# Kernel tuning notes

Measured on AMD Instinct MI355X. Metric: run time of the kernel, lower is better.

The kernel has to match this reference:

```python
import jax, jax.numpy as jnp
import numpy as np

TREE_DEPTH = 6
NUM_TREES = 64
NUM_LEAVES = 2 ** TREE_DEPTH
INPUT_DIM = 256
BATCH = 32768
BN_EPS = 1e-5


def _leaf_codes():
    # [L, depth] binary codes, MSB first (matches format(i, '0{depth}b'))
    i = np.arange(NUM_LEAVES)
    bits = (i[:, None] >> np.arange(TREE_DEPTH - 1, -1, -1)[None, :]) & 1
    return jnp.asarray(bits, dtype=jnp.float32)


def setup_inputs() -> dict:
    key = jax.random.key(0)
    ks = jax.random.split(key, 6)
    s = 1.0 / np.sqrt(INPUT_DIM)
    return {
        "x": jax.random.normal(ks[0], (BATCH, INPUT_DIM), jnp.float32),
        "W_dec": jax.random.normal(ks[1], (NUM_TREES, TREE_DEPTH, INPUT_DIM), jnp.float32) * s,
        "b_dec": jax.random.normal(ks[2], (NUM_TREES, TREE_DEPTH), jnp.float32) * s,
        "leaf_values": jax.random.normal(ks[3], (NUM_TREES, NUM_LEAVES), jnp.float32),
        "bn_gamma": jnp.ones((NUM_TREES,), jnp.float32),
        "bn_beta": jnp.zeros((NUM_TREES,), jnp.float32),
        "bn_mean": jnp.zeros((NUM_TREES,), jnp.float32),
        "bn_var": jnp.ones((NUM_TREES,), jnp.float32),
        "fc_w": jax.random.normal(ks[4], (INPUT_DIM, NUM_TREES), jnp.float32) / np.sqrt(NUM_TREES),
        "fc_b": jnp.zeros((INPUT_DIM,), jnp.float32),
    }


def reference(x, W_dec, b_dec, leaf_values, bn_gamma, bn_beta, bn_mean, bn_var, fc_w, fc_b):
    # Decision probabilities for all trees at once: [B, T, depth]
    dec = jax.nn.sigmoid(jnp.einsum("bd,tkd->btk", x, W_dec) + b_dec)
    codes = _leaf_codes()  # [L, depth]
    # Leaf probabilities: product over depth of (dec*code + (1-dec)*(1-code)).
    # Loop over the small fixed depth to avoid a [B,T,L,depth] intermediate.
    probs = jnp.ones((x.shape[0], NUM_TREES, NUM_LEAVES), x.dtype)
    for d in range(TREE_DEPTH):
        dd = dec[:, :, d][:, :, None]            # [B, T, 1]
        c = codes[:, d]                          # [L]
        probs = probs * (dd * c + (1.0 - dd) * (1.0 - c))
    # Weighted sum of leaf values per tree: [B, T]
    tree_out = jnp.einsum("btl,tl->bt", probs, leaf_values)
    # BatchNorm1d in eval mode (running stats), dropout is identity in eval.
    tree_out = (tree_out - bn_mean) * jax.lax.rsqrt(bn_var + BN_EPS) * bn_gamma + bn_beta
    # Final projection back to input_dim: [B, D]
    return tree_out @ fc_w.T + fc_b
```

## Files before the change

kernel.cpp:

```cpp
#include <hip/hip_runtime.h>
#include <hip/hip_bf16.h>

typedef __attribute__((ext_vector_type(8))) short short8;
typedef __attribute__((ext_vector_type(4))) float floatx4;

#define LOG2E 1.4426950408889634f

__device__ __forceinline__ unsigned short f2bf(float f) {
  unsigned int u = __float_as_uint(f);
  u += 0x7FFFu + ((u >> 16) & 1u);
  return (unsigned short)(u >> 16);
}

__device__ __forceinline__ unsigned int pk2(float lo, float hi) {
  __hip_bfloat162 h = __float22bfloat162_rn(make_float2(lo, hi));
  unsigned int u;
  __builtin_memcpy(&u, &h, 4);
  return u;
}

__global__ void prep_kernel(const float* __restrict__ W_dec,
                            const float* __restrict__ b_dec,
                            const float* __restrict__ leaf,
                            const float* __restrict__ bn_gamma,
                            const float* __restrict__ bn_beta,
                            const float* __restrict__ bn_mean,
                            const float* __restrict__ bn_var,
                            const float* __restrict__ fc_w,
                            unsigned short* __restrict__ Wp,
                            unsigned short* __restrict__ fcw,
                            float* __restrict__ coefg,
                            float* __restrict__ b1)
{
  int idx = (int)blockIdx.x * 256 + (int)threadIdx.x;
  if (idx < 384 * 256) {
    int np = idx >> 8, k = idx & 255;
    int d = np >> 6, t = np & 63;
    Wp[idx] = f2bf(-LOG2E * W_dec[(t * 6 + d) * 256 + k]);
    return;
  }
  idx -= 384 * 256;
  if (idx < 256 * 64) { fcw[idx] = f2bf(fc_w[idx]); return; }
  idx -= 256 * 64;
  if (idx < 64) {
    const int t = idx;
    float c[64];
    #pragma unroll
    for (int i = 0; i < 64; ++i) c[i] = leaf[t * 64 + i];
    #pragma unroll
    for (int p = 0; p < 6; ++p) {
      const int s = 1 << p;
      #pragma unroll
      for (int i = 0; i < 64; ++i)
        if ((i & s) == 0) c[i + s] -= c[i];
    }
    float sbv = bn_gamma[t] * rsqrtf(bn_var[t] + 1e-5f);
    float obv = bn_beta[t] - bn_mean[t] * sbv;
    #pragma unroll
    for (int i = 0; i < 64; ++i) c[i] *= sbv;
    c[0] += obv;
    #pragma unroll
    for (int i = 0; i < 64; ++i) coefg[t * 64 + i] = c[i];
    return;
  }
  idx -= 64;
  if (idx < 384) {
    int t = idx / 6, d = idx % 6;
    b1[d * 64 + t] = -LOG2E * b_dec[idx];
  }
}

__global__ __launch_bounds__(256, 3)
void node_main(const float* __restrict__ x,
               const unsigned short* __restrict__ Wp,
               const unsigned short* __restrict__ fcw,
               const float* __restrict__ coefg,
               const float* __restrict__ b1g,
               const float* __restrict__ fc_b,
               float* __restrict__ out)
{
  __shared__ __align__(16) char smem[36864];
  unsigned short (*xbf)[264] = (unsigned short (*)[264])smem;
  unsigned short (*A2)[72]   = (unsigned short (*)[72])smem;
  float (*coef_lds)[68]      = (float (*)[68])(smem + 16896);
  float* b1_lds              = (float*)(smem + 34304);
  float* fcb_lds             = (float*)(smem + 35840);

  const int tid  = (int)threadIdx.x;
  const int lane = tid & 63;
  const int w    = tid >> 6;
  const int tcol = lane & 15;
  const int g    = lane >> 4;
  const int r0   = (int)blockIdx.x * 32;

  {
    const float4* xs = (const float4*)(x + (size_t)r0 * 256);
    #pragma unroll
    for (int i = 0; i < 8; ++i) {
      int f = tid + 256 * i;
      float4 v = xs[f];
      int row = f >> 6, c4 = f & 63;
      unsigned int* p = (unsigned int*)&xbf[row][c4 * 4];
      p[0] = pk2(v.x, v.y);
      p[1] = pk2(v.z, v.w);
    }
    #pragma unroll
    for (int i = 0; i < 4; ++i) {
      int f = tid + 256 * i;
      int t = f >> 4, c4 = f & 15;
      *(float4*)&coef_lds[t][c4 * 4] = ((const float4*)coefg)[f];
    }
    b1_lds[tid] = b1g[tid];
    if (tid < 128) b1_lds[256 + tid] = b1g[256 + tid];
    fcb_lds[tid] = fc_b[tid];
  }
  __syncthreads();

  floatx4 acc[2][6];
  #pragma unroll
  for (int rt = 0; rt < 2; ++rt)
    #pragma unroll
    for (int d = 0; d < 6; ++d) { acc[rt][d][0]=0.f; acc[rt][d][1]=0.f; acc[rt][d][2]=0.f; acc[rt][d][3]=0.f; }

  const unsigned short* Bb = Wp + (size_t)(w * 16 + tcol) * 256 + g * 8;

  #pragma unroll
  for (int kp = 0; kp < 8; ++kp) {
    short8 b[6];
    #pragma unroll
    for (int d = 0; d < 6; ++d) b[d] = *(const short8*)(Bb + d * 16384 + kp * 32);
    short8 a0 = *(const short8*)&xbf[tcol][kp * 32 + g * 8];
    short8 a1 = *(const short8*)&xbf[16 + tcol][kp * 32 + g * 8];
    #pragma unroll
    for (int d = 0; d < 6; ++d) {
      acc[0][d] = __builtin_amdgcn_mfma_f32_16x16x32_bf16(a0, b[d], acc[0][d], 0, 0, 0);
      acc[1][d] = __builtin_amdgcn_mfma_f32_16x16x32_bf16(a1, b[d], acc[1][d], 0, 0, 0);
    }
  }
  __syncthreads();

  const int tree = w * 16 + tcol;
  float bp[6];
  #pragma unroll
  for (int d = 0; d < 6; ++d) bp[d] = b1_lds[d * 64 + tree];

  #pragma unroll
  for (int rt = 0; rt < 2; ++rt)
    #pragma unroll
    for (int d = 0; d < 6; ++d)
      #pragma unroll
      for (int j = 0; j < 4; ++j) {
        float z = acc[rt][d][j] + bp[d];
        acc[rt][d][j] = __builtin_amdgcn_rcpf(1.0f + __builtin_amdgcn_exp2f(z));
      }

  float L[32], resLo[8];
  #pragma unroll
  for (int c = 0; c < 8; ++c) {
    float4 v = *(const float4*)&coef_lds[tree][c * 4];
    L[c*4+0] = v.x; L[c*4+1] = v.y; L[c*4+2] = v.z; L[c*4+3] = v.w;
  }
  #pragma unroll
  for (int rt = 0; rt < 2; ++rt)
    #pragma unroll
    for (int j = 0; j < 4; ++j) {
      float u[16];
      const float d5 = acc[rt][5][j];
      #pragma unroll
      for (int i = 0; i < 16; ++i) u[i] = fmaf(d5, L[2*i+1], L[2*i]);
      const float d4 = acc[rt][4][j];
      #pragma unroll
      for (int i = 0; i < 8; ++i) u[i] = fmaf(d4, u[2*i+1], u[2*i]);
      const float d3 = acc[rt][3][j];
      #pragma unroll
      for (int i = 0; i < 4; ++i) u[i] = fmaf(d3, u[2*i+1], u[2*i]);
      const float d2 = acc[rt][2][j];
      #pragma unroll
      for (int i = 0; i < 2; ++i) u[i] = fmaf(d2, u[2*i+1], u[2*i]);
      resLo[rt*4+j] = fmaf(acc[rt][1][j], u[1], u[0]);
    }
  #pragma unroll
  for (int c = 0; c < 8; ++c) {
    float4 v = *(const float4*)&coef_lds[tree][32 + c * 4];
    L[c*4+0] = v.x; L[c*4+1] = v.y; L[c*4+2] = v.z; L[c*4+3] = v.w;
  }
  #pragma unroll
  for (int rt = 0; rt < 2; ++rt)
    #pragma unroll
    for (int j = 0; j < 4; ++j) {
      float u[16];
      const float d5 = acc[rt][5][j];
      #pragma unroll
      for (int i = 0; i < 16; ++i) u[i] = fmaf(d5, L[2*i+1], L[2*i]);
      const float d4 = acc[rt][4][j];
      #pragma unroll
      for (int i = 0; i < 8; ++i) u[i] = fmaf(d4, u[2*i+1], u[2*i]);
      const float d3 = acc[rt][3][j];
      #pragma unroll
      for (int i = 0; i < 4; ++i) u[i] = fmaf(d3, u[2*i+1], u[2*i]);
      const float d2 = acc[rt][2][j];
      #pragma unroll
      for (int i = 0; i < 2; ++i) u[i] = fmaf(d2, u[2*i+1], u[2*i]);
      float hi_r = fmaf(acc[rt][1][j], u[1], u[0]);
      float to   = fmaf(acc[rt][0][j], hi_r, resLo[rt*4+j]);
      A2[rt * 16 + g * 4 + j][tree] = f2bf(to);
    }
  __syncthreads();

  floatx4 acc2[2][4];
  #pragma unroll
  for (int rt = 0; rt < 2; ++rt)
    #pragma unroll
    for (int nt = 0; nt < 4; ++nt) { acc2[rt][nt][0]=0.f; acc2[rt][nt][1]=0.f; acc2[rt][nt][2]=0.f; acc2[rt][nt][3]=0.f; }

  #pragma unroll
  for (int kst = 0; kst < 2; ++kst) {
    short8 a2[2];
    #pragma unroll
    for (int rt = 0; rt < 2; ++rt)
      a2[rt] = *(const short8*)&A2[rt * 16 + tcol][kst * 32 + g * 8];
    #pragma unroll
    for (int nt = 0; nt < 4; ++nt) {
      short8 b2 = *(const short8*)(fcw + (size_t)(w * 64 + nt * 16 + tcol) * 64 + kst * 32 + g * 8);
      #pragma unroll
      for (int rt = 0; rt < 2; ++rt)
        acc2[rt][nt] = __builtin_amdgcn_mfma_f32_16x16x32_bf16(a2[rt], b2, acc2[rt][nt], 0, 0, 0);
    }
  }

  #pragma unroll
  for (int nt = 0; nt < 4; ++nt) {
    const int col = w * 64 + nt * 16 + tcol;
    const float bv = fcb_lds[col];
    #pragma unroll
    for (int rt = 0; rt < 2; ++rt)
      #pragma unroll
      for (int j = 0; j < 4; ++j)
        out[(size_t)(r0 + rt * 16 + g * 4 + j) * 256 + col] = acc2[rt][nt][j] + bv;
  }
}

extern "C" void kernel_launch(void* const* d_in, const int* in_sizes, int n_in,
                              void* d_out, int out_size, void* d_ws, size_t ws_size,
                              hipStream_t stream) {
  const float* x        = (const float*)d_in[0];
  const float* W_dec    = (const float*)d_in[1];
  const float* b_dec    = (const float*)d_in[2];
  const float* leaf     = (const float*)d_in[3];
  const float* bn_gamma = (const float*)d_in[4];
  const float* bn_beta  = (const float*)d_in[5];
  const float* bn_mean  = (const float*)d_in[6];
  const float* bn_var   = (const float*)d_in[7];
  const float* fc_w     = (const float*)d_in[8];
  const float* fc_b     = (const float*)d_in[9];
  float* out = (float*)d_out;

  char* ws = (char*)d_ws;
  unsigned short* Wp  = (unsigned short*)(ws);
  unsigned short* fcw = (unsigned short*)(ws + 196608);
  float* coefg = (float*)(ws + 229376);
  float* b1    = (float*)(ws + 245760);

  prep_kernel<<<450, 256, 0, stream>>>(W_dec, b_dec, leaf, bn_gamma, bn_beta,
                                       bn_mean, bn_var, fc_w,
                                       Wp, fcw, coefg, b1);
  node_main<<<1024, 256, 0, stream>>>(x, Wp, fcw, coefg, b1, fc_b, out);
}
```

Before: 45.72 us.

## Double-buffer decision weights into LDS via async global_load_lds and vectorize prep

Decision-weight tiles are now streamed into a double-buffered LDS region with global_load_lds DMA, prefetching the next k-slice while the current one feeds the MFMAs, with a barrier per k-step. Leaf coefficients, biases and fc weights are loaded straight from global into registers instead of being staged through LDS. The prep kernel is vectorized to float4 and uses fewer blocks. Per-block LDS grows to about 66KB and launch bounds drop to 2 blocks per CU, trading occupancy and adding eight barriers for fewer global loads in the inner loop.

```diff
diff --git a/kernel.cpp b/kernel.cpp
--- a/kernel.cpp
+++ b/kernel.cpp
@@ -5,6 +5,8 @@
 typedef __attribute__((ext_vector_type(4))) float floatx4;
 
 #define LOG2E 1.4426950408889634f
+#define AS1 __attribute__((address_space(1)))
+#define AS3 __attribute__((address_space(3)))
 
 __device__ __forceinline__ unsigned short f2bf(float f) {
   unsigned int u = __float_as_uint(f);
@@ -17,6 +19,10 @@
   unsigned int u;
   __builtin_memcpy(&u, &h, 4);
   return u;
+}
+
+__device__ __forceinline__ void dma16(const void* g, void* l) {
+  __builtin_amdgcn_global_load_lds((const AS1 void*)g, (AS3 void*)l, 16, 0, 0);
 }
 
 __global__ void prep_kernel(const float* __restrict__ W_dec,
@@ -30,18 +36,28 @@
                             unsigned short* __restrict__ Wp,
                             unsigned short* __restrict__ fcw,
                             float* __restrict__ coefg,
-                            float* __restrict__ b1)
+                            float* __restrict__ b1t)
 {
   int idx = (int)blockIdx.x * 256 + (int)threadIdx.x;
-  if (idx < 384 * 256) {
-    int np = idx >> 8, k = idx & 255;
+  if (idx < 24576) {
+    int np = idx >> 6, k4 = (idx & 63) * 4;
     int d = np >> 6, t = np & 63;
-    Wp[idx] = f2bf(-LOG2E * W_dec[(t * 6 + d) * 256 + k]);
+    float4 v = *(const float4*)(W_dec + (size_t)(t * 6 + d) * 256 + k4);
+    ushort4 r;
+    r.x = f2bf(-LOG2E * v.x); r.y = f2bf(-LOG2E * v.y);
+    r.z = f2bf(-LOG2E * v.z); r.w = f2bf(-LOG2E * v.w);
+    *(ushort4*)(Wp + (size_t)np * 256 + k4) = r;
     return;
   }
-  idx -= 384 * 256;
-  if (idx < 256 * 64) { fcw[idx] = f2bf(fc_w[idx]); return; }
-  idx -= 256 * 64;
+  idx -= 24576;
+  if (idx < 4096) {
+    float4 v = *(const float4*)(fc_w + idx * 4);
+    ushort4 r;
+    r.x = f2bf(v.x); r.y = f2bf(v.y); r.z = f2bf(v.z); r.w = f2bf(v.w);
+    *(ushort4*)(fcw + idx * 4) = r;
+    return;
+  }
+  idx -= 4096;
   if (idx < 64) {
     const int t = idx;
     float c[64];
@@ -64,27 +80,25 @@
     return;
   }
   idx -= 64;
-  if (idx < 384) {
-    int t = idx / 6, d = idx % 6;
-    b1[d * 64 + t] = -LOG2E * b_dec[idx];
-  }
-}
-
-__global__ __launch_bounds__(256, 3)
+  if (idx < 512) {
+    int t = idx >> 3, d = idx & 7;
+    b1t[idx] = (d < 6) ? (-LOG2E * b_dec[t * 6 + d]) : 0.0f;
+  }
+}
+
+__global__ __launch_bounds__(256, 2)
 void node_main(const float* __restrict__ x,
                const unsigned short* __restrict__ Wp,
                const unsigned short* __restrict__ fcw,
                const float* __restrict__ coefg,
-               const float* __restrict__ b1g,
+               const float* __restrict__ b1t,
                const float* __restrict__ fc_b,
                float* __restrict__ out)
 {
-  __shared__ __align__(16) char smem[36864];
-  unsigned short (*xbf)[264] = (unsigned short (*)[264])smem;
-  unsigned short (*A2)[72]   = (unsigned short (*)[72])smem;
-  float (*coef_lds)[68]      = (float (*)[68])(smem + 16896);
-  float* b1_lds              = (float*)(smem + 34304);
-  float* fcb_lds             = (float*)(smem + 35840);
+  __shared__ __align__(1024) char smem[66048];
+  char* bufB = smem;
+  unsigned short (*xbf)[264] = (unsigned short (*)[264])(smem + 49152);
+  unsigned short (*A2)[72]   = (unsigned short (*)[72])(smem + 49152);
 
   const int tid  = (int)threadIdx.x;
   const int lane = tid & 63;
@@ -92,6 +106,18 @@
   const int tcol = lane & 15;
   const int g    = lane >> 4;
   const int r0   = (int)blockIdx.x * 32;
+  const int tree = w * 16 + tcol;
+
+  const unsigned short* Ws = Wp + (size_t)lane * 256;
+  {
+    char* base = bufB + w * 1024;
+    #pragma unroll
+    for (int i = 0; i < 6; ++i) {
+      int gd = i * 4 + w;
+      int d = gd % 6, gg = gd / 6;
+      dma16(Ws + d * 16384 + gg * 8, base + i * 4096);
+    }
+  }
 
   {
     const float4* xs = (const float4*)(x + (size_t)r0 * 256);
@@ -104,17 +130,10 @@
       p[0] = pk2(v.x, v.y);
       p[1] = pk2(v.z, v.w);
     }
-    #pragma unroll
-    for (int i = 0; i < 4; ++i) {
-      int f = tid + 256 * i;
-      int t = f >> 4, c4 = f & 15;
-      *(float4*)&coef_lds[t][c4 * 4] = ((const float4*)coefg)[f];
-    }
-    b1_lds[tid] = b1g[tid];
-    if (tid < 128) b1_lds[256 + tid] = b1g[256 + tid];
-    fcb_lds[tid] = fc_b[tid];
-  }
-  __syncthreads();
+  }
+  asm volatile("s_waitcnt vmcnt(0) lgkmcnt(0)" ::: "memory");
+  __builtin_amdgcn_s_barrier();
+  __builtin_amdgcn_sched_barrier(0);
 
   floatx4 acc[2][6];
   #pragma unroll
@@ -122,13 +141,24 @@
     #pragma unroll
     for (int d = 0; d < 6; ++d) { acc[rt][d][0]=0.f; acc[rt][d][1]=0.f; acc[rt][d][2]=0.f; acc[rt][d][3]=0.f; }
 
-  const unsigned short* Bb = Wp + (size_t)(w * 16 + tcol) * 256 + g * 8;
-
   #pragma unroll
   for (int kp = 0; kp < 8; ++kp) {
+    const int cur = kp & 1;
+    if (kp + 1 < 8) {
+      char* base = bufB + (cur ^ 1) * 24576 + w * 1024;
+      const unsigned short* s0 = Ws + (kp + 1) * 32;
+      #pragma unroll
+      for (int i = 0; i < 6; ++i) {
+        int gd = i * 4 + w;
+        int d = gd % 6, gg = gd / 6;
+        dma16(s0 + d * 16384 + gg * 8, base + i * 4096);
+      }
+    }
+    const char* cb = bufB + cur * 24576;
     short8 b[6];
     #pragma unroll
-    for (int d = 0; d < 6; ++d) b[d] = *(const short8*)(Bb + d * 16384 + kp * 32);
+    for (int d = 0; d < 6; ++d)
+      b[d] = *(const short8*)(cb + (size_t)(((g * 6 + d) * 64) + tree) * 16);
     short8 a0 = *(const short8*)&xbf[tcol][kp * 32 + g * 8];
     short8 a1 = *(const short8*)&xbf[16 + tcol][kp * 32 + g * 8];
     #pragma unroll
@@ -136,14 +166,28 @@
       acc[0][d] = __builtin_amdgcn_mfma_f32_16x16x32_bf16(a0, b[d], acc[0][d], 0, 0, 0);
       acc[1][d] = __builtin_amdgcn_mfma_f32_16x16x32_bf16(a1, b[d], acc[1][d], 0, 0, 0);
     }
-  }
-  __syncthreads();
-
-  const int tree = w * 16 + tcol;
-  float bp[6];
-  #pragma unroll
-  for (int d = 0; d < 6; ++d) bp[d] = b1_lds[d * 64 + tree];
-
+    asm volatile("s_waitcnt vmcnt(0) lgkmcnt(0)" ::: "memory");
+    __builtin_amdgcn_s_barrier();
+    __builtin_amdgcn_sched_barrier(0);
+  }
+
+  const float* Ct = coefg + tree * 64;
+  float4 q0 = *(const float4*)(b1t + tree * 8);
+  float4 q1 = *(const float4*)(b1t + tree * 8 + 4);
+  float4 lv[8];
+  #pragma unroll
+  for (int c = 0; c < 8; ++c) lv[c] = ((const float4*)Ct)[c];
+  short8 B2[2][4];
+  float fcb[4];
+  #pragma unroll
+  for (int nt = 0; nt < 4; ++nt) {
+    const unsigned short* p = fcw + (size_t)(w * 64 + nt * 16 + tcol) * 64 + g * 8;
+    B2[0][nt] = *(const short8*)p;
+    B2[1][nt] = *(const short8*)(p + 32);
+    fcb[nt] = fc_b[w * 64 + nt * 16 + tcol];
+  }
+
+  float bp[6] = {q0.x, q0.y, q0.z, q0.w, q1.x, q1.y};
   #pragma unroll
   for (int rt = 0; rt < 2; ++rt)
     #pragma unroll
@@ -157,9 +201,12 @@
   float L[32], resLo[8];
   #pragma unroll
   for (int c = 0; c < 8; ++c) {
-    float4 v = *(const float4*)&coef_lds[tree][c * 4];
-    L[c*4+0] = v.x; L[c*4+1] = v.y; L[c*4+2] = v.z; L[c*4+3] = v.w;
-  }
+    L[c*4+0] = lv[c].x; L[c*4+1] = lv[c].y; L[c*4+2] = lv[c].z; L[c*4+3] = lv[c].w;
+  }
+  float4 hv[8];
+  #pragma unroll
+  for (int c = 0; c < 8; ++c) hv[c] = ((const float4*)Ct)[8 + c];
+
   #pragma unroll
   for (int rt = 0; rt < 2; ++rt)
     #pragma unroll
@@ -181,8 +228,7 @@
     }
   #pragma unroll
   for (int c = 0; c < 8; ++c) {
-    float4 v = *(const float4*)&coef_lds[tree][32 + c * 4];
-    L[c*4+0] = v.x; L[c*4+1] = v.y; L[c*4+2] = v.z; L[c*4+3] = v.w;
+    L[c*4+0] = hv[c].x; L[c*4+1] = hv[c].y; L[c*4+2] = hv[c].z; L[c*4+3] = hv[c].w;
   }
   #pragma unroll
   for (int rt = 0; rt < 2; ++rt)
@@ -202,8 +248,8 @@
       #pragma unroll
       for (int i = 0; i < 2; ++i) u[i] = fmaf(d2, u[2*i+1], u[2*i]);
       float hi_r = fmaf(acc[rt][1][j], u[1], u[0]);
-      float to   = fmaf(acc[rt][0][j], hi_r, resLo[rt*4+j]);
-      A2[rt * 16 + g * 4 + j][tree] = f2bf(to);
+      float tov  = fmaf(acc[rt][0][j], hi_r, resLo[rt*4+j]);
+      A2[rt * 16 + g * 4 + j][tree] = f2bf(tov);
     }
   __syncthreads();
 
@@ -220,23 +266,20 @@
     for (int rt = 0; rt < 2; ++rt)
       a2[rt] = *(const short8*)&A2[rt * 16 + tcol][kst * 32 + g * 8];
     #pragma unroll
-    for (int nt = 0; nt < 4; ++nt) {
-      short8 b2 = *(const short8*)(fcw + (size_t)(w * 64 + nt * 16 + tcol) * 64 + kst * 32 + g * 8);
+    for (int nt = 0; nt < 4; ++nt)
       #pragma unroll
       for (int rt = 0; rt < 2; ++rt)
-        acc2[rt][nt] = __builtin_amdgcn_mfma_f32_16x16x32_bf16(a2[rt], b2, acc2[rt][nt], 0, 0, 0);
-    }
+        acc2[rt][nt] = __builtin_amdgcn_mfma_f32_16x16x32_bf16(a2[rt], B2[kst][nt], acc2[rt][nt], 0, 0, 0);
   }
 
   #pragma unroll
   for (int nt = 0; nt < 4; ++nt) {
     const int col = w * 64 + nt * 16 + tcol;
-    const float bv = fcb_lds[col];
     #pragma unroll
     for (int rt = 0; rt < 2; ++rt)
       #pragma unroll
       for (int j = 0; j < 4; ++j)
-        out[(size_t)(r0 + rt * 16 + g * 4 + j) * 256 + col] = acc2[rt][nt][j] + bv;
+        out[(size_t)(r0 + rt * 16 + g * 4 + j) * 256 + col] = acc2[rt][nt][j] + fcb[nt];
   }
 }
 
@@ -259,10 +302,10 @@
   unsigned short* Wp  = (unsigned short*)(ws);
   unsigned short* fcw = (unsigned short*)(ws + 196608);
   float* coefg = (float*)(ws + 229376);
-  float* b1    = (float*)(ws + 245760);
-
-  prep_kernel<<<450, 256, 0, stream>>>(W_dec, b_dec, leaf, bn_gamma, bn_beta,
+  float* b1t   = (float*)(ws + 245760);
+
+  prep_kernel<<<115, 256, 0, stream>>>(W_dec, b_dec, leaf, bn_gamma, bn_beta,
                                        bn_mean, bn_var, fc_w,
-                                       Wp, fcw, coefg, b1);
-  node_main<<<1024, 256, 0, stream>>>(x, Wp, fcw, coefg, b1, fc_b, out);
-}
+                                       Wp, fcw, coefg, b1t);
+  node_main<<<1024, 256, 0, stream>>>(x, Wp, fcw, coefg, b1t, fc_b, out);
+}
```

Result: slower. 64.16 us (+40.3%).
